# Kernel optimization log

Measured on AMD Instinct MI355X. Metric: run time of the kernel, lower is better.

The kernel has to match this reference:

```python
import jax, jax.numpy as jnp
import numpy as np

N = 50000       # nodes
E = 1600000     # edges (avg degree 32)
IN = 64         # in_channels
ED = 16         # edge_dim
H = 128         # hidden_channels


def setup_inputs() -> dict:
    key = jax.random.key(0)
    ks = jax.random.split(key, 32)
    rn = lambda k, shape, s: jax.random.normal(k, shape, jnp.float32) * s
    inp = {}
    inp['x'] = rn(ks[0], (N, IN), 1.0)
    inp['edge_index'] = jax.random.randint(ks[1], (2, E), 0, N, dtype=jnp.int64)
    inp['edge_attr'] = rn(ks[2], (E, ED), 1.0)
    # per-layer params: edge linear (ED -> node_dim), MLP (d_in->H, H->H)
    node_dims = [IN, H, H]
    i = 3
    for l, d in enumerate(node_dims):
        inp[f'We{l}'] = rn(ks[i], (ED, d), 1.0 / np.sqrt(ED)); i += 1
        inp[f'be{l}'] = jnp.zeros((d,), jnp.float32)
        inp[f'W1_{l}'] = rn(ks[i], (d, H), 1.0 / np.sqrt(d)); i += 1
        inp[f'b1_{l}'] = jnp.zeros((H,), jnp.float32)
        inp[f'W2_{l}'] = rn(ks[i], (H, H), 1.0 / np.sqrt(H)); i += 1
        inp[f'b2_{l}'] = jnp.zeros((H,), jnp.float32)
    inp['Wlin'] = rn(ks[i], (H, 1), 1.0 / np.sqrt(H))
    inp['blin'] = jnp.zeros((1,), jnp.float32)
    return inp


def gine_conv(x, src, dst, ea, We, be, W1, b1, W2, b2):
    # message: relu(x_j + Lin_e(edge_attr)); aggregate: sum into dst; eps=0
    msg = jax.nn.relu(x[src] + ea @ We + be)            # [E, d]
    agg = jax.ops.segment_sum(msg, dst, num_segments=x.shape[0])  # [N, d]
    h = x + agg                                          # (1+eps)*x + agg, eps=0
    return jax.nn.relu(h @ W1 + b1) @ W2 + b2            # MLP


def reference(x, edge_index, edge_attr,
              We0, be0, W1_0, b1_0, W2_0, b2_0,
              We1, be1, W1_1, b1_1, W2_1, b2_1,
              We2, be2, W1_2, b1_2, W2_2, b2_2,
              Wlin, blin):
    src, dst = edge_index[0], edge_index[1]
    h = jax.nn.relu(gine_conv(x, src, dst, edge_attr, We0, be0, W1_0, b1_0, W2_0, b2_0))
    h = jax.nn.relu(gine_conv(h, src, dst, edge_attr, We1, be1, W1_1, b1_1, W2_1, b2_1))
    h = jax.nn.relu(gine_conv(h, src, dst, edge_attr, We2, be2, W1_2, b1_2, W2_2, b2_2))
    out = jax.nn.sigmoid(h @ Wlin + blin)                # [N, 1]
    return out.squeeze(-1)                               # [N]
```

## Files before the change

kernel.cpp:

```cpp
#include <hip/hip_runtime.h>
#include <math.h>


#define BLK 256

typedef __attribute__((ext_vector_type(2))) float f32x2;

__device__ inline f32x2 pk_fma(f32x2 a, f32x2 b, f32x2 c) {
    f32x2 d;
    asm("v_pk_fma_f32 %0, %1, %2, %3" : "=v"(d) : "v"(a), "v"(b), "v"(c));
    return d;
}


__global__ void detect_kernel(const unsigned int* __restrict__ ei, int* __restrict__ flag) {
    int t = blockIdx.x * blockDim.x + threadIdx.x;
    if (t < 1024) {
        if (ei[2 * t + 1] != 0u) atomicOr(flag, 1);
    }
}

__global__ void convert_hist_kernel(const int* __restrict__ ei32, const long long* __restrict__ ei64,
                                    const int* __restrict__ flag, int E,
                                    int* __restrict__ src, int* __restrict__ dst,
                                    int* __restrict__ counts) {
    int e = blockIdx.x * blockDim.x + threadIdx.x;
    if (e >= E) return;
    int s, d;
    if (*flag) { s = ei32[e]; d = ei32[E + e]; }
    else       { s = (int)ei64[e]; d = (int)ei64[E + e]; }
    src[e] = s; dst[e] = d;
    atomicAdd(&counts[d], 1);
}

__global__ void scan_kernel(const int* __restrict__ counts, int* __restrict__ offsets, int n) {
    __shared__ int tsum[256];
    __shared__ int texcl[256];
    int t = threadIdx.x;
    int chunk = (n + 255) >> 8;
    int b = t * chunk, e = min(b + chunk, n);
    int s = 0;
    for (int i = b; i < e; i++) s += counts[i];
    tsum[t] = s;
    __syncthreads();
    if (t == 0) {
        int run = 0;
        for (int i = 0; i < 256; i++) { texcl[i] = run; run += tsum[i]; }
        offsets[n] = run;
    }
    __syncthreads();
    int run = texcl[t];
    for (int i = b; i < e; i++) { offsets[i] = run; run += counts[i]; }
}

__global__ void scatter_ea_kernel(const int* __restrict__ src, const int* __restrict__ dst,
                                  const int* __restrict__ offsets, int* __restrict__ cursor,
                                  const float4* __restrict__ ea4,
                                  int* __restrict__ srcp, float4* __restrict__ eap4, int E) {
    int e = blockIdx.x * blockDim.x + threadIdx.x;
    if (e >= E) return;
    int d = dst[e];
    int pos = offsets[d] + atomicAdd(&cursor[d], 1);
    srcp[pos] = src[e];
    float4 a = ea4[(size_t)e * 4 + 0], b = ea4[(size_t)e * 4 + 1];
    float4 c = ea4[(size_t)e * 4 + 2], w = ea4[(size_t)e * 4 + 3];
    eap4[(size_t)pos * 4 + 0] = a;
    eap4[(size_t)pos * 4 + 1] = b;
    eap4[(size_t)pos * 4 + 2] = c;
    eap4[(size_t)pos * 4 + 3] = w;
}

template <int D>
__global__ __launch_bounds__(256) void aggregate_kernel(
    const float* __restrict__ x, const float* __restrict__ eap,
    const int* __restrict__ srcp,
    const float* __restrict__ We, const float* __restrict__ be,
    const int* __restrict__ offsets,
    float* __restrict__ h, int n) {
    constexpr int C = D / 64;
    int lane = threadIdx.x & 63;
    int node = __builtin_amdgcn_readfirstlane(blockIdx.x * 4 + (threadIdx.x >> 6));
    if (node >= n) return;
    int c0 = lane * C;

    f32x2 wp[C][8];
#pragma unroll
    for (int j = 0; j < C; j++)
#pragma unroll
        for (int t = 0; t < 8; t++) {
            f32x2 v; v.x = We[(2 * t) * D + c0 + j]; v.y = We[(2 * t + 1) * D + c0 + j];
            wp[j][t] = v;
        }
    float bias[C], acc[C];
#pragma unroll
    for (int j = 0; j < C; j++) {
        bias[j] = be[c0 + j];
        acc[j] = x[(size_t)node * D + c0 + j];
    }
    int p = offsets[node], pe = offsets[node + 1];

    for (; p + 4 <= pe; p += 4) {
        int s0 = srcp[p], s1 = srcp[p + 1], s2 = srcp[p + 2], s3 = srcp[p + 3];
        float xv[4][C];
        {
            const float* r0 = x + (size_t)s0 * D + c0;
            const float* r1 = x + (size_t)s1 * D + c0;
            const float* r2 = x + (size_t)s2 * D + c0;
            const float* r3 = x + (size_t)s3 * D + c0;
            if constexpr (C == 2) {
                float2 t0 = *(const float2*)r0, t1 = *(const float2*)r1;
                float2 t2 = *(const float2*)r2, t3 = *(const float2*)r3;
                xv[0][0] = t0.x; xv[0][1] = t0.y; xv[1][0] = t1.x; xv[1][1] = t1.y;
                xv[2][0] = t2.x; xv[2][1] = t2.y; xv[3][0] = t3.x; xv[3][1] = t3.y;
            } else {
                xv[0][0] = *r0; xv[1][0] = *r1; xv[2][0] = *r2; xv[3][0] = *r3;
            }
        }
#pragma unroll
        for (int u = 0; u < 4; u++) {
            const float4* er = (const float4*)(eap + (size_t)(p + u) * 16);
            float4 e0 = er[0], e1 = er[1], e2 = er[2], e3 = er[3];
            f32x2 ev[8];
            ev[0].x = e0.x; ev[0].y = e0.y;  ev[1].x = e0.z; ev[1].y = e0.w;
            ev[2].x = e1.x; ev[2].y = e1.y;  ev[3].x = e1.z; ev[3].y = e1.w;
            ev[4].x = e2.x; ev[4].y = e2.y;  ev[5].x = e2.z; ev[5].y = e2.w;
            ev[6].x = e3.x; ev[6].y = e3.y;  ev[7].x = e3.z; ev[7].y = e3.w;
#pragma unroll
            for (int j = 0; j < C; j++) {
                f32x2 prod; prod.x = xv[u][j] + bias[j]; prod.y = 0.f;
#pragma unroll
                for (int t = 0; t < 8; t++) prod = pk_fma(ev[t], wp[j][t], prod);
                acc[j] += fmaxf(prod.x + prod.y, 0.f);
            }
        }
    }
    for (; p < pe; p++) {
        int s = srcp[p];
        const float* xr = x + (size_t)s * D + c0;
        float xv[C];
        if constexpr (C == 2) { float2 t = *(const float2*)xr; xv[0] = t.x; xv[1] = t.y; }
        else xv[0] = *xr;
        const float4* er = (const float4*)(eap + (size_t)p * 16);
        float4 e0 = er[0], e1 = er[1], e2 = er[2], e3 = er[3];
        f32x2 ev[8];
        ev[0].x = e0.x; ev[0].y = e0.y;  ev[1].x = e0.z; ev[1].y = e0.w;
        ev[2].x = e1.x; ev[2].y = e1.y;  ev[3].x = e1.z; ev[3].y = e1.w;
        ev[4].x = e2.x; ev[4].y = e2.y;  ev[5].x = e2.z; ev[5].y = e2.w;
        ev[6].x = e3.x; ev[6].y = e3.y;  ev[7].x = e3.z; ev[7].y = e3.w;
#pragma unroll
        for (int j = 0; j < C; j++) {
            f32x2 prod; prod.x = xv[j] + bias[j]; prod.y = 0.f;
#pragma unroll
            for (int t = 0; t < 8; t++) prod = pk_fma(ev[t], wp[j][t], prod);
            acc[j] += fmaxf(prod.x + prod.y, 0.f);
        }
    }
#pragma unroll
    for (int j = 0; j < C; j++) h[(size_t)node * D + c0 + j] = acc[j];
}

template <int K>
__global__ __launch_bounds__(256) void gemm_kernel(
    const float* __restrict__ A, const float* __restrict__ B,
    const float* __restrict__ bias, float* __restrict__ C, int n) {
    __shared__ __align__(16) float As[16][68];
    __shared__ __align__(16) float Bs[16][128];
    int t = threadIdx.x;
    int row0 = blockIdx.x * 64;
    int tr = t >> 5, tc = t & 31;
    float acc[8][4];
#pragma unroll
    for (int r = 0; r < 8; r++)
#pragma unroll
        for (int c = 0; c < 4; c++) acc[r][c] = 0.f;

    int lr = t >> 2, lk = (t & 3) * 4;
    int bk = t >> 4, bc = (t & 15) * 8;

    for (int ks = 0; ks < K; ks += 16) {
        float4 a;
        int grow = row0 + lr;
        if (grow < n) a = *(const float4*)(A + (size_t)grow * K + ks + lk);
        else a = make_float4(0.f, 0.f, 0.f, 0.f);
        As[lk + 0][lr] = a.x; As[lk + 1][lr] = a.y;
        As[lk + 2][lr] = a.z; As[lk + 3][lr] = a.w;

        const float4* bp = (const float4*)(B + (size_t)(ks + bk) * 128 + bc);
        float4 b0 = bp[0], b1 = bp[1];
        *(float4*)&Bs[bk][bc] = b0;
        *(float4*)&Bs[bk][bc + 4] = b1;
        __syncthreads();
#pragma unroll
        for (int kk = 0; kk < 16; kk++) {
            float4 a0 = *(const float4*)&As[kk][tr * 8];
            float4 a1 = *(const float4*)&As[kk][tr * 8 + 4];
            float4 bv = *(const float4*)&Bs[kk][tc * 4];
            float ar[8] = {a0.x, a0.y, a0.z, a0.w, a1.x, a1.y, a1.z, a1.w};
            float bc4[4] = {bv.x, bv.y, bv.z, bv.w};
#pragma unroll
            for (int r = 0; r < 8; r++)
#pragma unroll
                for (int c = 0; c < 4; c++) acc[r][c] = fmaf(ar[r], bc4[c], acc[r][c]);
        }
        __syncthreads();
    }
    float4 bb = *(const float4*)(bias + tc * 4);
#pragma unroll
    for (int r = 0; r < 8; r++) {
        int grow = row0 + tr * 8 + r;
        if (grow < n) {
            float4 v;
            v.x = fmaxf(acc[r][0] + bb.x, 0.f);
            v.y = fmaxf(acc[r][1] + bb.y, 0.f);
            v.z = fmaxf(acc[r][2] + bb.z, 0.f);
            v.w = fmaxf(acc[r][3] + bb.w, 0.f);
            *(float4*)(C + (size_t)grow * 128 + tc * 4) = v;
        }
    }
}

__global__ __launch_bounds__(256) void final_kernel(
    const float* __restrict__ x, const float* __restrict__ Wlin,
    const float* __restrict__ blin, float* __restrict__ out, int n) {
    int lane = threadIdx.x & 63;
    int node = blockIdx.x * 4 + (threadIdx.x >> 6);
    if (node >= n) return;
    float2 w = *(const float2*)(Wlin + lane * 2);
    float2 xv = *(const float2*)(x + (size_t)node * 128 + lane * 2);
    float v = xv.x * w.x + xv.y * w.y;
#pragma unroll
    for (int off = 32; off; off >>= 1) v += __shfl_down(v, off, 64);
    if (lane == 0) out[node] = 1.f / (1.f + expf(-(v + blin[0])));
}

extern "C" void kernel_launch(void* const* d_in, const int* in_sizes, int n_in,
                              void* d_out, int out_size, void* d_ws, size_t ws_size,
                              hipStream_t stream) {
    const float* x_in = (const float*)d_in[0];
    const void* ei    = d_in[1];
    const float* ea   = (const float*)d_in[2];
    const float* We[3]  = {(const float*)d_in[3], (const float*)d_in[9],  (const float*)d_in[15]};
    const float* be[3]  = {(const float*)d_in[4], (const float*)d_in[10], (const float*)d_in[16]};
    const float* W1[3]  = {(const float*)d_in[5], (const float*)d_in[11], (const float*)d_in[17]};
    const float* b1[3]  = {(const float*)d_in[6], (const float*)d_in[12], (const float*)d_in[18]};
    const float* W2[3]  = {(const float*)d_in[7], (const float*)d_in[13], (const float*)d_in[19]};
    const float* b2[3]  = {(const float*)d_in[8], (const float*)d_in[14], (const float*)d_in[20]};
    const float* Wlin = (const float*)d_in[21];
    const float* blin = (const float*)d_in[22];
    float* out = (float*)d_out;

    const int N = in_sizes[0] / 64;
    const int E = in_sizes[1] / 2;

    size_t off = 0;
    auto alloc = [&](size_t bytes) {
        void* p = (char*)d_ws + off;
        off += (bytes + 255) & ~(size_t)255;
        return p;
    };
    int*   flag    = (int*)alloc(4);
    int*   src32   = (int*)alloc((size_t)E * 4);
    int*   dst32   = (int*)alloc((size_t)E * 4);
    int*   counts  = (int*)alloc((size_t)N * 4);
    int*   offsets = (int*)alloc((size_t)(N + 1) * 4);
    int*   cursor  = (int*)alloc((size_t)N * 4);
    int*   srcp    = (int*)alloc((size_t)E * 4);
    float* eap     = (float*)alloc((size_t)E * 16 * 4);
    float* bufA    = (float*)alloc((size_t)N * 128 * 4);
    float* bufB    = (float*)alloc((size_t)N * 128 * 4);
    float* bufC    = (float*)alloc((size_t)N * 128 * 4);

    hipMemsetAsync(flag, 0, 4, stream);
    hipMemsetAsync(counts, 0, (size_t)N * 4, stream);
    hipMemsetAsync(cursor, 0, (size_t)N * 4, stream);

    int egrid = (E + BLK - 1) / BLK;
    detect_kernel<<<4, BLK, 0, stream>>>((const unsigned int*)ei, flag);
    convert_hist_kernel<<<egrid, BLK, 0, stream>>>((const int*)ei, (const long long*)ei, flag, E,
                                                   src32, dst32, counts);
    scan_kernel<<<1, BLK, 0, stream>>>(counts, offsets, N);
    scatter_ea_kernel<<<egrid, BLK, 0, stream>>>(src32, dst32, offsets, cursor,
                                                 (const float4*)ea, srcp, (float4*)eap, E);

    int ngrid4 = (N + 3) / 4;
    int ggrid  = (N + 63) / 64;

    aggregate_kernel<64><<<ngrid4, BLK, 0, stream>>>(x_in, eap, srcp, We[0], be[0], offsets, bufA, N);
    gemm_kernel<64><<<ggrid, BLK, 0, stream>>>(bufA, W1[0], b1[0], bufB, N);
    gemm_kernel<128><<<ggrid, BLK, 0, stream>>>(bufB, W2[0], b2[0], bufC, N);
    aggregate_kernel<128><<<ngrid4, BLK, 0, stream>>>(bufC, eap, srcp, We[1], be[1], offsets, bufA, N);
    gemm_kernel<128><<<ggrid, BLK, 0, stream>>>(bufA, W1[1], b1[1], bufB, N);
    gemm_kernel<128><<<ggrid, BLK, 0, stream>>>(bufB, W2[1], b2[1], bufC, N);
    aggregate_kernel<128><<<ngrid4, BLK, 0, stream>>>(bufC, eap, srcp, We[2], be[2], offsets, bufA, N);
    gemm_kernel<128><<<ggrid, BLK, 0, stream>>>(bufA, W1[2], b1[2], bufB, N);
    gemm_kernel<128><<<ggrid, BLK, 0, stream>>>(bufB, W2[2], b2[2], bufC, N);

    final_kernel<<<ngrid4, BLK, 0, stream>>>(bufC, Wlin, blin, out, N);
}
```

Measured before the change: 993.6 us.

## Capture edge rank in histogram atomic and gather edge attributes via permutation

The histogram kernel now keeps the value returned by its atomicAdd as each edge's rank within its destination bucket. It packs that rank with the destination id into one 32-bit word, which removes the second atomic pass and the cursor memset. The CSR build then scatters only a 4-byte permutation index. A separate kernel, using four threads per edge, gathers source ids and 64-byte edge attributes in sorted order, so scattered writes become coalesced writes with scattered reads. The packing assumes node ids and per-node degree both fit in 16 bits, which holds for N=50000 but not for larger graphs.

```diff
diff --git a/kernel.cpp b/kernel.cpp
--- a/kernel.cpp
+++ b/kernel.cpp
@@ -22,15 +22,16 @@
 
 __global__ void convert_hist_kernel(const int* __restrict__ ei32, const long long* __restrict__ ei64,
                                     const int* __restrict__ flag, int E,
-                                    int* __restrict__ src, int* __restrict__ dst,
+                                    int* __restrict__ src, unsigned int* __restrict__ drank,
                                     int* __restrict__ counts) {
     int e = blockIdx.x * blockDim.x + threadIdx.x;
     if (e >= E) return;
     int s, d;
     if (*flag) { s = ei32[e]; d = ei32[E + e]; }
     else       { s = (int)ei64[e]; d = (int)ei64[E + e]; }
-    src[e] = s; dst[e] = d;
-    atomicAdd(&counts[d], 1);
+    src[e] = s;
+    unsigned int r = (unsigned int)atomicAdd(&counts[d], 1);
+    drank[e] = (unsigned int)d | (r << 16);
 }
 
 __global__ void scan_kernel(const int* __restrict__ counts, int* __restrict__ offsets, int n) {
@@ -53,21 +54,25 @@
     for (int i = b; i < e; i++) { offsets[i] = run; run += counts[i]; }
 }
 
-__global__ void scatter_ea_kernel(const int* __restrict__ src, const int* __restrict__ dst,
-                                  const int* __restrict__ offsets, int* __restrict__ cursor,
-                                  const float4* __restrict__ ea4,
-                                  int* __restrict__ srcp, float4* __restrict__ eap4, int E) {
+__global__ void scatter_perm_kernel(const unsigned int* __restrict__ drank,
+                                    const int* __restrict__ offsets,
+                                    int* __restrict__ perm, int E) {
     int e = blockIdx.x * blockDim.x + threadIdx.x;
     if (e >= E) return;
-    int d = dst[e];
-    int pos = offsets[d] + atomicAdd(&cursor[d], 1);
-    srcp[pos] = src[e];
-    float4 a = ea4[(size_t)e * 4 + 0], b = ea4[(size_t)e * 4 + 1];
-    float4 c = ea4[(size_t)e * 4 + 2], w = ea4[(size_t)e * 4 + 3];
-    eap4[(size_t)pos * 4 + 0] = a;
-    eap4[(size_t)pos * 4 + 1] = b;
-    eap4[(size_t)pos * 4 + 2] = c;
-    eap4[(size_t)pos * 4 + 3] = w;
+    unsigned int v = drank[e];
+    perm[offsets[v & 0xffffu] + (int)(v >> 16)] = e;
+}
+
+__global__ __launch_bounds__(256) void gather_ea_kernel(
+    const int* __restrict__ perm, const int* __restrict__ src32,
+    const float4* __restrict__ ea4,
+    int* __restrict__ srcp, float4* __restrict__ eap4, int E) {
+    int t = blockIdx.x * blockDim.x + threadIdx.x;
+    int p = t >> 2, q = t & 3;
+    if (p >= E) return;
+    int e = perm[p];
+    if (q == 0) srcp[p] = src32[e];
+    eap4[(size_t)p * 4 + q] = ea4[(size_t)e * 4 + q];
 }
 
 template <int D>
@@ -258,29 +263,30 @@
         off += (bytes + 255) & ~(size_t)255;
         return p;
     };
-    int*   flag    = (int*)alloc(4);
-    int*   src32   = (int*)alloc((size_t)E * 4);
-    int*   dst32   = (int*)alloc((size_t)E * 4);
-    int*   counts  = (int*)alloc((size_t)N * 4);
-    int*   offsets = (int*)alloc((size_t)(N + 1) * 4);
-    int*   cursor  = (int*)alloc((size_t)N * 4);
-    int*   srcp    = (int*)alloc((size_t)E * 4);
-    float* eap     = (float*)alloc((size_t)E * 16 * 4);
-    float* bufA    = (float*)alloc((size_t)N * 128 * 4);
-    float* bufB    = (float*)alloc((size_t)N * 128 * 4);
-    float* bufC    = (float*)alloc((size_t)N * 128 * 4);
+    int*          flag    = (int*)alloc(4);
+    int*          src32   = (int*)alloc((size_t)E * 4);
+    unsigned int* drank   = (unsigned int*)alloc((size_t)E * 4);
+    int*          counts  = (int*)alloc((size_t)N * 4);
+    int*          offsets = (int*)alloc((size_t)(N + 1) * 4);
+    int*          perm    = (int*)alloc((size_t)E * 4);
+    int*          srcp    = (int*)alloc((size_t)E * 4);
+    float*        eap     = (float*)alloc((size_t)E * 16 * 4);
+    float*        bufA    = (float*)alloc((size_t)N * 128 * 4);
+    float*        bufB    = (float*)alloc((size_t)N * 128 * 4);
+    float*        bufC    = (float*)alloc((size_t)N * 128 * 4);
 
     hipMemsetAsync(flag, 0, 4, stream);
     hipMemsetAsync(counts, 0, (size_t)N * 4, stream);
-    hipMemsetAsync(cursor, 0, (size_t)N * 4, stream);
 
     int egrid = (E + BLK - 1) / BLK;
     detect_kernel<<<4, BLK, 0, stream>>>((const unsigned int*)ei, flag);
     convert_hist_kernel<<<egrid, BLK, 0, stream>>>((const int*)ei, (const long long*)ei, flag, E,
-                                                   src32, dst32, counts);
+                                                   src32, drank, counts);
     scan_kernel<<<1, BLK, 0, stream>>>(counts, offsets, N);
-    scatter_ea_kernel<<<egrid, BLK, 0, stream>>>(src32, dst32, offsets, cursor,
-                                                 (const float4*)ea, srcp, (float4*)eap, E);
+    scatter_perm_kernel<<<egrid, BLK, 0, stream>>>(drank, offsets, perm, E);
+    int g4grid = ((E * 4) + BLK - 1) / BLK;
+    gather_ea_kernel<<<g4grid, BLK, 0, stream>>>(perm, src32, (const float4*)ea,
+                                                 srcp, (float4*)eap, E);
 
     int ngrid4 = (N + 3) / 4;
     int ggrid  = (N + 63) / 64;
```

Result: faster. 945.0 us (-4.9%).
